# Kernel optimization log

Hardware: AMD Instinct MI355X
Metric: run time of the kernel (lower is better)

## Reference

```python
import jax, jax.numpy as jnp
import numpy as np

N_PF, N_GW, N_SW = 60000, 300000, 60000
D_IN, D, E = 32, 64, 1_000_000


def _mk_edge(key, n_src, n_dst, n_edges):
    k1, k2 = jax.random.split(key)
    return jnp.stack([
        jax.random.randint(k1, (n_edges,), 0, n_src),
        jax.random.randint(k2, (n_edges,), 0, n_dst),
    ]).astype(jnp.int32)


def _self_edge(n):
    r = jnp.arange(n, dtype=jnp.int32)
    return jnp.stack([r, r])


def setup_inputs() -> dict:
    key = jax.random.key(0)
    ks = jax.random.split(key, 20)
    s = 0.05
    return {
        "x_pf": jax.random.normal(ks[0], (N_PF, D_IN), jnp.float32),
        "x_gw": jax.random.normal(ks[1], (N_GW, D_IN), jnp.float32),
        "x_sw": jax.random.normal(ks[2], (N_SW, D_IN), jnp.float32),
        "W1l": jax.random.normal(ks[3], (10, D, D_IN), jnp.float32) * s,
        "b1l": jax.random.normal(ks[4], (10, D), jnp.float32) * s,
        "W1r": jax.random.normal(ks[5], (10, D, D_IN), jnp.float32) * s,
        "W2l": jax.random.normal(ks[6], (10, D, D), jnp.float32) * s,
        "b2l": jax.random.normal(ks[7], (10, D), jnp.float32) * s,
        "W2r": jax.random.normal(ks[8], (10, D, D), jnp.float32) * s,
        "lin_W": jax.random.normal(ks[9], (1, D), jnp.float32) * s,
        "lin_b": jax.random.normal(ks[10], (1,), jnp.float32) * s,
        "prelu_a": jnp.float32(0.25),
        "ei_pf_gw": _mk_edge(ks[11], N_PF, N_GW, E),
        "ei_gw_pf": _mk_edge(ks[12], N_GW, N_PF, E),
        "ei_pf_sw": _mk_edge(ks[13], N_PF, N_SW, E),
        "ei_sw_pf": _mk_edge(ks[14], N_SW, N_PF, E),
        "ei_sw_gw": _mk_edge(ks[15], N_SW, N_GW, E),
        "ei_gw_sw": _mk_edge(ks[16], N_GW, N_SW, E),
        "ei_gw_gw": _mk_edge(ks[17], N_GW, N_GW, E),
        "ei_gw_self": _self_edge(N_GW),
        "ei_sw_self": _self_edge(N_SW),
        "ei_pf_self": _self_edge(N_PF),
    }


def reference(x_pf, x_gw, x_sw, W1l, b1l, W1r, W2l, b2l, W2r, lin_W, lin_b,
              prelu_a, ei_pf_gw, ei_gw_pf, ei_pf_sw, ei_sw_pf, ei_sw_gw,
              ei_gw_sw, ei_gw_gw, ei_gw_self, ei_sw_self, ei_pf_self):
    n_pf, n_gw, n_sw = x_pf.shape[0], x_gw.shape[0], x_sw.shape[0]

    def sage(x_src, x_dst, ei, Wl, bl, Wr, n_dst):
        # PyG SAGEConv: lin_l(mean_j x_j) + lin_r(x_i); lin_r has no bias
        msg = x_src[ei[0]]                                        # [E, Din]
        summed = jax.ops.segment_sum(msg, ei[1], num_segments=n_dst)
        cnt = jax.ops.segment_sum(jnp.ones(ei.shape[1], x_src.dtype), ei[1],
                                  num_segments=n_dst)
        mean = summed / jnp.maximum(cnt, 1.0)[:, None]            # [Ndst, Din]
        return mean @ Wl.T + bl + x_dst @ Wr.T

    def layer(h_pf, h_gw, h_sw, Wl, bl, Wr):
        # HeteroConv with aggr='sum' over edge types per destination node type
        out_gw = (sage(h_pf, h_gw, ei_pf_gw, Wl[0], bl[0], Wr[0], n_gw)
                  + sage(h_sw, h_gw, ei_sw_gw, Wl[4], bl[4], Wr[4], n_gw)
                  + sage(h_gw, h_gw, ei_gw_gw, Wl[6], bl[6], Wr[6], n_gw)
                  + sage(h_gw, h_gw, ei_gw_self, Wl[7], bl[7], Wr[7], n_gw))
        out_pf = (sage(h_gw, h_pf, ei_gw_pf, Wl[1], bl[1], Wr[1], n_pf)
                  + sage(h_sw, h_pf, ei_sw_pf, Wl[3], bl[3], Wr[3], n_pf)
                  + sage(h_pf, h_pf, ei_pf_self, Wl[9], bl[9], Wr[9], n_pf))
        out_sw = (sage(h_pf, h_sw, ei_pf_sw, Wl[2], bl[2], Wr[2], n_sw)
                  + sage(h_gw, h_sw, ei_gw_sw, Wl[5], bl[5], Wr[5], n_sw)
                  + sage(h_sw, h_sw, ei_sw_self, Wl[8], bl[8], Wr[8], n_sw))
        return out_pf, out_gw, out_sw

    h_pf, h_gw, h_sw = layer(x_pf, x_gw, x_sw, W1l, b1l, W1r)
    h_pf, h_gw, h_sw = jax.nn.relu(h_pf), jax.nn.relu(h_gw), jax.nn.relu(h_sw)
    h_pf, h_gw, h_sw = layer(h_pf, h_gw, h_sw, W2l, b2l, W2r)
    h_pf, h_gw, h_sw = jax.nn.relu(h_pf), jax.nn.relu(h_gw), jax.nn.relu(h_sw)

    def prelu(v):
        return jnp.where(v >= 0, v, prelu_a * v)

    out_gw = prelu(h_gw @ lin_W.T + lin_b)   # [N_GW, 1]
    out_sw = prelu(h_sw @ lin_W.T + lin_b)   # [N_SW, 1]
    return out_gw, out_sw, h_pf
```

## Files before the change

### kernel.cpp

```cpp
#include <hip/hip_runtime.h>

typedef __attribute__((ext_vector_type(8))) short short8;
typedef __attribute__((ext_vector_type(4))) float floatx4;

#define N_PF 60000
#define N_GW 300000
#define N_SW 60000
#define EPT 1000000
#define TOTE 7000000
#define L_CNT 1140000
#define SPAN 4096
#define N_B 279
#define CHSZ 4096
#define NCH 1709

__device__ __forceinline__ unsigned short f2bf(float f) {
  unsigned u = __float_as_uint(f);
  u = (u + 0x7FFF + ((u >> 16) & 1)) >> 16;
  return (unsigned short)u;
}
__device__ __forceinline__ float bf2f(unsigned short u) {
  return __uint_as_float((unsigned)u << 16);
}
__device__ __forceinline__ void acc8(float* a, short8 v) {
#pragma unroll
  for (int k = 0; k < 8; ++k) a[k] += bf2f((unsigned short)v[k]);
}

__device__ __forceinline__ int cnt_base(int et) {
  switch (et) {
    case 0: return 0;
    case 1: return 300000;
    case 2: return 360000;
    case 3: return 420000;
    case 4: return 480000;
    case 5: return 780000;
    default: return 840000;
  }
}

__device__ __forceinline__ const int* pick(const int* e0, const int* e1,
                                           const int* e2, const int* e3,
                                           const int* e4, const int* e5,
                                           const int* e6, int et) {
  switch (et) {
    case 0: return e0; case 1: return e1; case 2: return e2; case 3: return e3;
    case 4: return e4; case 5: return e5; default: return e6;
  }
}

__global__ __launch_bounds__(256) void k_cast(const float4* __restrict__ x,
                                              ushort4* __restrict__ xb, int n4) {
  int i = blockIdx.x * 256 + threadIdx.x;
  if (i < n4) {
    float4 v = x[i];
    ushort4 o;
    o.x = f2bf(v.x); o.y = f2bf(v.y); o.z = f2bf(v.z); o.w = f2bf(v.w);
    xb[i] = o;
  }
}


__global__ __launch_bounds__(256) void k_h1(
    const int* e0, const int* e1, const int* e2, const int* e3,
    const int* e4, const int* e5, const int* e6, int* __restrict__ hcnt) {
  __shared__ int hist[N_B];
  int ch = blockIdx.x, t = threadIdx.x;
  for (int i = t; i < N_B; i += 256) hist[i] = 0;
  __syncthreads();
  int base = ch * CHSZ;
  int nn = TOTE - base; if (nn > CHSZ) nn = CHSZ;
#pragma unroll
  for (int u = 0; u < CHSZ / 256; ++u) {
    int o = u * 256 + t;
    if (o < nn) {
      int gid = base + o;
      int et = gid / EPT, i2 = gid - et * EPT;
      const int* ei = pick(e0, e1, e2, e3, e4, e5, e6, et);
      int idx = cnt_base(et) + ei[EPT + i2];
      atomicAdd(&hist[idx >> 12], 1);
    }
  }
  __syncthreads();
  for (int b = t; b < N_B; b += 256) hcnt[(size_t)b * NCH + ch] = hist[b];
}

__global__ __launch_bounds__(256) void k_h2a(const int* __restrict__ hcnt,
                                             int* __restrict__ btot) {
  __shared__ int sh[4];
  int b = blockIdx.x;
  const int* c = hcnt + (size_t)b * NCH;
  int s = 0;
  for (int k = threadIdx.x; k < NCH; k += 256) s += c[k];
  for (int off = 1; off < 64; off <<= 1) s += __shfl_xor(s, off, 64);
  int lane = threadIdx.x & 63, w = threadIdx.x >> 6;
  if (lane == 0) sh[w] = s;
  __syncthreads();
  if (threadIdx.x == 0) btot[b] = sh[0] + sh[1] + sh[2] + sh[3];
}

__global__ __launch_bounds__(64) void k_h2b(const int* __restrict__ btot,
                                            int* __restrict__ bbase,
                                            int* __restrict__ Sarr) {
  int lane = threadIdx.x;
  int v[5]; int s = 0;
#pragma unroll
  for (int k = 0; k < 5; ++k) {
    int i = lane * 5 + k;
    v[k] = (i < N_B) ? btot[i] : 0;
    s += v[k];
  }
  int x = s;
  for (int off = 1; off < 64; off <<= 1) {
    int tv = __shfl_up(x, off, 64);
    if (lane >= off) x += tv;
  }
  int run = x - s;
#pragma unroll
  for (int k = 0; k < 5; ++k) {
    int i = lane * 5 + k;
    if (i < N_B) bbase[i] = run;
    run += v[k];
  }
  if (lane == 63) { bbase[N_B] = x; Sarr[L_CNT] = TOTE; }
}

__global__ __launch_bounds__(256) void k_h2c(int* __restrict__ hcnt,
                                             const int* __restrict__ bbase) {
  __shared__ int sc[256];
  int b = blockIdx.x, t = threadIdx.x;
  int* c = hcnt + (size_t)b * NCH;
  int v[7]; int s = 0;
#pragma unroll
  for (int k = 0; k < 7; ++k) {
    int i = t * 7 + k;
    v[k] = (i < NCH) ? c[i] : 0;
    s += v[k];
  }
  sc[t] = s;
  __syncthreads();
  for (int off = 1; off < 256; off <<= 1) {
    int tv = (t >= off) ? sc[t - off] : 0;
    __syncthreads();
    sc[t] += tv;
    __syncthreads();
  }
  int run = bbase[b] + sc[t] - s;
#pragma unroll
  for (int k = 0; k < 7; ++k) {
    int i = t * 7 + k;
    if (i < NCH) { int vv = v[k]; c[i] = run; run += vv; }
  }
}

__global__ __launch_bounds__(256) void k_bfill(
    const int* e0, const int* e1, const int* e2, const int* e3,
    const int* e4, const int* e5, const int* e6,
    const int* __restrict__ hcnt, unsigned* __restrict__ part) {
  __shared__ int hist[N_B];
  __shared__ int segs[N_B];
  __shared__ int curb[N_B];
  __shared__ int gbase[N_B];
  __shared__ int sc[256];
  __shared__ unsigned long long stg[CHSZ];
  int ch = blockIdx.x, t = threadIdx.x;
  for (int i = t; i < N_B; i += 256) hist[i] = 0;
  __syncthreads();
  int base = ch * CHSZ;
  int nn = TOTE - base; if (nn > CHSZ) nn = CHSZ;
#pragma unroll
  for (int u = 0; u < CHSZ / 256; ++u) {
    int o = u * 256 + t;
    if (o < nn) {
      int gid = base + o;
      int et = gid / EPT, i2 = gid - et * EPT;
      const int* ei = pick(e0, e1, e2, e3, e4, e5, e6, et);
      int idx = cnt_base(et) + ei[EPT + i2];
      atomicAdd(&hist[idx >> 12], 1);
    }
  }
  __syncthreads();
  int v0 = (2 * t < N_B) ? hist[2 * t] : 0;
  int v1 = (2 * t + 1 < N_B) ? hist[2 * t + 1] : 0;
  int s = v0 + v1;
  sc[t] = s;
  __syncthreads();
  for (int off = 1; off < 256; off <<= 1) {
    int tv = (t >= off) ? sc[t - off] : 0;
    __syncthreads();
    sc[t] += tv;
    __syncthreads();
  }
  int excl = sc[t] - s;
  if (2 * t < N_B) { segs[2 * t] = excl; curb[2 * t] = excl; }
  if (2 * t + 1 < N_B) { segs[2 * t + 1] = excl + v0; curb[2 * t + 1] = excl + v0; }
  for (int b = t; b < N_B; b += 256) gbase[b] = hcnt[(size_t)b * NCH + ch];
  __syncthreads();
#pragma unroll
  for (int u = 0; u < CHSZ / 256; ++u) {
    int o = u * 256 + t;
    if (o < nn) {
      int gid = base + o;
      int et = gid / EPT, i2 = gid - et * EPT;
      const int* ei = pick(e0, e1, e2, e3, e4, e5, e6, et);
      int dst = ei[EPT + i2];
      int src = ei[i2];
      int idx = cnt_base(et) + dst;
      unsigned long long p = ((unsigned long long)idx << 32) | (unsigned)src;
      int r = atomicAdd(&curb[idx >> 12], 1);
      stg[r] = p;
    }
  }
  __syncthreads();
  for (int sdx = t; sdx < nn; sdx += 256) {
    unsigned long long p = stg[sdx];
    int idx = (int)(p >> 32);
    int b = idx >> 12;
    unsigned ent = ((unsigned)(idx & 4095) << 19) | (unsigned)(p & 0x7FFFF);
    part[(size_t)gbase[b] + (sdx - segs[b])] = ent;
  }
}

__global__ __launch_bounds__(1024) void k_cfill(
    const unsigned* __restrict__ part, const int* __restrict__ bbase,
    int* __restrict__ Sarr, int* __restrict__ col) {
  __shared__ int hist[SPAN];
  __shared__ int wt[16];
  int t = threadIdx.x;
  int lane = t & 63, wv = t >> 6;
  int b = blockIdx.x;
  int lo = b * SPAN;
  int span_n = L_CNT - lo; if (span_n > SPAN) span_n = SPAN;
  int s0 = bbase[b], s1 = bbase[b + 1];
  ((int4*)hist)[t] = (int4){0, 0, 0, 0};
  __syncthreads();
  for (int j = s0 + t; j < s1; j += 1024) {
    int local = (int)(part[j] >> 19);
    atomicAdd(&hist[local], 1);
  }
  __syncthreads();
  int4 v = ((int4*)hist)[t];
  int s = v.x + v.y + v.z + v.w;
  int x = s;
#pragma unroll
  for (int off = 1; off < 64; off <<= 1) {
    int tv = __shfl_up(x, off, 64);
    if (lane >= off) x += tv;
  }
  if (lane == 63) wt[wv] = x;
  __syncthreads();
  int woff = 0;
#pragma unroll
  for (int k = 0; k < 16; ++k) woff += (k < wv) ? wt[k] : 0;
  int run = woff + x - s;
  int4 cur4, sa4;
  cur4.x = run; sa4.x = s0 + run; run += v.x;
  cur4.y = run; sa4.y = s0 + run; run += v.y;
  cur4.z = run; sa4.z = s0 + run; run += v.z;
  cur4.w = run; sa4.w = s0 + run; run += v.w;
  __syncthreads();
  ((int4*)hist)[t] = cur4;
  if (t * 4 + 3 < span_n) {
    *(int4*)(&Sarr[lo + t * 4]) = sa4;
  } else {
    if (t * 4 + 0 < span_n) Sarr[lo + t * 4 + 0] = sa4.x;
    if (t * 4 + 1 < span_n) Sarr[lo + t * 4 + 1] = sa4.y;
    if (t * 4 + 2 < span_n) Sarr[lo + t * 4 + 2] = sa4.z;
  }
  __syncthreads();
  for (int j = s0 + t; j < s1; j += 1024) {
    unsigned p = part[j];
    int local = (int)(p >> 19);
    int r = atomicAdd(&hist[local], 1);
    col[s0 + r] = (int)(p & 0x7FFFF);
  }
}

template <int KIN, int NE>
__global__ __launch_bounds__(256) void k_prep(
    const float* __restrict__ Wl, const float* __restrict__ Wr,
    const float* __restrict__ bl, int e0, int e1, int e2, int es,
    unsigned short* __restrict__ wsw, float* __restrict__ bias) {
  constexpr int KCAT = (NE + 1) * KIN;
  int idx = blockIdx.x * 256 + threadIdx.x;
  if (idx < KCAT * 64) {
    int j = idx & 7, lane = (idx >> 3) & 63, t = idx >> 9;
    int ct = t & 3, kc = t >> 2;
    int k = kc * 32 + ((lane >> 4) << 3) + j;
    int c = ct * 16 + (lane & 15);
    int seg = k / KIN, kk = k - seg * KIN;
    float v;
    if (seg < NE) {
      int e = (seg == 0) ? e0 : (seg == 1) ? e1 : e2;
      v = Wl[((size_t)e * 64 + c) * KIN + kk];
    } else {
      v = Wl[((size_t)es * 64 + c) * KIN + kk] +
          Wr[((size_t)es * 64 + c) * KIN + kk] +
          Wr[((size_t)e0 * 64 + c) * KIN + kk] +
          Wr[((size_t)e1 * 64 + c) * KIN + kk];
      if (NE == 3) v += Wr[((size_t)e2 * 64 + c) * KIN + kk];
    }
    wsw[idx] = f2bf(v);
  } else if (idx < KCAT * 64 + 64) {
    int c = idx - KCAT * 64;
    float v = bl[e0 * 64 + c] + bl[e1 * 64 + c] + bl[es * 64 + c];
    if (NE == 3) v += bl[e2 * 64 + c];
    bias[c] = v;
  }
}

struct LType {
  const unsigned short* s0;
  const unsigned short* s1;
  const unsigned short* s2;
  int b0, b1, b2, ne;
  const unsigned short* xD;
  const unsigned short* wsw;
  const float* bias;
  void* hOut;
  int omode;
  int ntile;
};

template <int KIN, int MINW>
__global__ __launch_bounds__(256, MINW) void k_layerF(
    const int* __restrict__ Sarr, const int* __restrict__ col, LType t0,
    LType t1, LType t2, const float* __restrict__ linW,
    const float* __restrict__ linb, const float* __restrict__ pa) {
  constexpr int ZSTR = 3 * KIN + 8;
  constexpr int LPR = KIN / 8;
  constexpr int G = 64 / LPR;
  constexpr int KD = KIN / 32;
  __shared__ unsigned short z[4 * 16 * ZSTR];
  const int lane = threadIdx.x & 63;
  unsigned short* zw = &z[(threadIdx.x >> 6) * 16 * ZSTR];
  const int wid = (blockIdx.x * 256 + threadIdx.x) >> 6;
  const int nw = (gridDim.x * 256) >> 6;
  const int cl = lane & 15, quad = lane >> 4;
  const int g = lane / LPR;
  const int c = lane % LPR;
  const int TT = t0.ntile + t1.ntile + t2.ntile;

  for (int tile = wid; tile < TT; tile += nw) {
    LType tp;
    int lt = tile;
    if (lt < t0.ntile) tp = t0;
    else if ((lt -= t0.ntile) < t1.ntile) tp = t1;
    else { lt -= t1.ntile; tp = t2; }
    const int nb = lt * 16;
    const int ne = tp.ne;
    const int klds = ne * KD;

    short8 adst[KD];
#pragma unroll
    for (int kd = 0; kd < KD; ++kd)
      adst[kd] = *(const short8*)(tp.xD + (size_t)(nb + cl) * KIN +
                                  kd * 32 + quad * 8);

#pragma unroll
    for (int i0 = 0; i0 < 16; i0 += G) {
      int n = nb + i0 + g;
      unsigned short* zr = &zw[(i0 + g) * ZSTR];
      int s0v = Sarr[tp.b0 + n], t0v = Sarr[tp.b0 + n + 1];
      int s1v = Sarr[tp.b1 + n], t1v = Sarr[tp.b1 + n + 1];
      int s2v = 0, t2v = 0;
      if (ne == 3) { s2v = Sarr[tp.b2 + n]; t2v = Sarr[tp.b2 + n + 1]; }
#pragma unroll
      for (int E = 0; E < 3; ++E) {
        if (E < ne) {
          const unsigned short* se =
              (E == 0) ? tp.s0 : (E == 1) ? tp.s1 : tp.s2;
          int s = (E == 0) ? s0v : (E == 1) ? s1v : s2v;
          int t = (E == 0) ? t0v : (E == 1) ? t1v : t2v;
          float a0[8] = {0, 0, 0, 0, 0, 0, 0, 0};
          float a1[8] = {0, 0, 0, 0, 0, 0, 0, 0};
          int j = s;
          for (; j + 1 < t; j += 2) {
            int r0 = col[j], r1 = col[j + 1];
            short8 v0 = *(const short8*)(se + (size_t)r0 * KIN + c * 8);
            short8 v1 = *(const short8*)(se + (size_t)r1 * KIN + c * 8);
            acc8(a0, v0);
            acc8(a1, v1);
          }
          if (j < t) {
            int r0 = col[j];
            short8 v0 = *(const short8*)(se + (size_t)r0 * KIN + c * 8);
            acc8(a0, v0);
          }
          int cv = t - s;
          if (cv < 1) cv = 1;
          float inv = 1.0f / (float)cv;
          short8 o;
#pragma unroll
          for (int k = 0; k < 8; ++k)
            o[k] = (short)f2bf((a0[k] + a1[k]) * inv);
          *(short8*)(&zr[E * KIN + c * 8]) = o;
        }
      }
    }
    floatx4 acc[4];
#pragma unroll
    for (int ct = 0; ct < 4; ++ct) {
      float bv = tp.bias[ct * 16 + cl];
      acc[ct] = (floatx4){bv, bv, bv, bv};
    }
    for (int kc = 0; kc < klds; ++kc) {
      short8 a = *(const short8*)(&zw[cl * ZSTR + kc * 32 + quad * 8]);
#pragma unroll
      for (int ct = 0; ct < 4; ++ct) {
        short8 b =
            *(const short8*)(tp.wsw + ((size_t)(kc * 4 + ct) * 64 + lane) * 8);
        acc[ct] = __builtin_amdgcn_mfma_f32_16x16x32_bf16(a, b, acc[ct], 0, 0, 0);
      }
    }
#pragma unroll
    for (int kd = 0; kd < KD; ++kd) {
      short8 a = adst[kd];
      int kc = klds + kd;
#pragma unroll
      for (int ct = 0; ct < 4; ++ct) {
        short8 b =
            *(const short8*)(tp.wsw + ((size_t)(kc * 4 + ct) * 64 + lane) * 8);
        acc[ct] = __builtin_amdgcn_mfma_f32_16x16x32_bf16(a, b, acc[ct], 0, 0, 0);
      }
    }
    if (tp.omode == 2) {
      float p[4] = {0.f, 0.f, 0.f, 0.f};
#pragma unroll
      for (int ct = 0; ct < 4; ++ct) {
        float w = linW[ct * 16 + cl];
#pragma unroll
        for (int r = 0; r < 4; ++r) {
          float v = acc[ct][r];
          v = v > 0.f ? v : 0.f;
          p[r] += v * w;
        }
      }
#pragma unroll
      for (int off = 1; off < 16; off <<= 1) {
#pragma unroll
        for (int r = 0; r < 4; ++r) p[r] += __shfl_xor(p[r], off, 64);
      }
      if (cl == 0) {
        float lb = linb[0], al = pa[0];
        float* o = (float*)tp.hOut;
#pragma unroll
        for (int r = 0; r < 4; ++r) {
          int n = nb + quad * 4 + r;
          float v = p[r] + lb;
          o[n] = v >= 0.f ? v : al * v;
        }
      }
    } else if (tp.omode == 1) {
#pragma unroll
      for (int ct = 0; ct < 4; ++ct)
#pragma unroll
        for (int r = 0; r < 4; ++r) {
          int n = nb + quad * 4 + r;
          float v = acc[ct][r];
          ((float*)tp.hOut)[(size_t)n * 64 + ct * 16 + cl] = v > 0.f ? v : 0.f;
        }
    } else {
#pragma unroll
      for (int ct = 0; ct < 4; ++ct)
#pragma unroll
        for (int r = 0; r < 4; ++r) {
          int n = nb + quad * 4 + r;
          float v = acc[ct][r];
          ((unsigned short*)tp.hOut)[(size_t)n * 64 + ct * 16 + cl] =
              f2bf(v > 0.f ? v : 0.f);
        }
    }
  }
}

extern "C" void kernel_launch(void* const* d_in, const int* in_sizes, int n_in,
                              void* d_out, int out_size, void* d_ws,
                              size_t ws_size, hipStream_t stream) {
  const float* x_pf = (const float*)d_in[0];
  const float* x_gw = (const float*)d_in[1];
  const float* x_sw = (const float*)d_in[2];
  const float* W1l = (const float*)d_in[3];
  const float* b1l = (const float*)d_in[4];
  const float* W1r = (const float*)d_in[5];
  const float* W2l = (const float*)d_in[6];
  const float* b2l = (const float*)d_in[7];
  const float* W2r = (const float*)d_in[8];
  const float* linW = (const float*)d_in[9];
  const float* linb = (const float*)d_in[10];
  const float* pa = (const float*)d_in[11];
  const int* e0 = (const int*)d_in[12];
  const int* e1 = (const int*)d_in[13];
  const int* e2 = (const int*)d_in[14];
  const int* e3 = (const int*)d_in[15];
  const int* e4 = (const int*)d_in[16];
  const int* e5 = (const int*)d_in[17];
  const int* e6 = (const int*)d_in[18];
  float* out = (float*)d_out;

  char* w = (char*)d_ws;
  size_t off = 0;
  auto alloc = [&](size_t bytes) -> void* {
    void* p = w + off;
    off += bytes;
    off = (off + 255) & ~(size_t)255;
    return p;
  };
  unsigned* part = (unsigned*)alloc((size_t)TOTE * 4);
  int* col = (int*)alloc((size_t)TOTE * 4);
  int* Sarr = (int*)alloc((size_t)(L_CNT + 1) * 4);
  int* hcnt = (int*)alloc((size_t)N_B * NCH * 4);
  int* btot = (int*)alloc((N_B + 1) * 4);
  int* bbase = (int*)alloc((N_B + 1) * 4);
  unsigned short* xb_pf = (unsigned short*)alloc((size_t)N_PF * 32 * 2);
  unsigned short* xb_gw = (unsigned short*)alloc((size_t)N_GW * 32 * 2);
  unsigned short* xb_sw = (unsigned short*)alloc((size_t)N_SW * 32 * 2);
  unsigned short* h1_pf = (unsigned short*)alloc((size_t)N_PF * 64 * 2);
  unsigned short* h1_gw = (unsigned short*)alloc((size_t)N_GW * 64 * 2);
  unsigned short* h1_sw = (unsigned short*)alloc((size_t)N_SW * 64 * 2);
  unsigned short* w1gw = (unsigned short*)alloc(128 * 64 * 2);
  unsigned short* w1pf = (unsigned short*)alloc(96 * 64 * 2);
  unsigned short* w1sw = (unsigned short*)alloc(96 * 64 * 2);
  unsigned short* w2gw = (unsigned short*)alloc(256 * 64 * 2);
  unsigned short* w2pf = (unsigned short*)alloc(192 * 64 * 2);
  unsigned short* w2sw = (unsigned short*)alloc(192 * 64 * 2);
  float* bs1gw = (float*)alloc(64 * 4);
  float* bs1pf = (float*)alloc(64 * 4);
  float* bs1sw = (float*)alloc(64 * 4);
  float* bs2gw = (float*)alloc(64 * 4);
  float* bs2pf = (float*)alloc(64 * 4);
  float* bs2sw = (float*)alloc(64 * 4);

  k_cast<<<(N_PF * 8 + 255) / 256, 256, 0, stream>>>((const float4*)x_pf,
                                                     (ushort4*)xb_pf, N_PF * 8);
  k_cast<<<(N_GW * 8 + 255) / 256, 256, 0, stream>>>((const float4*)x_gw,
                                                     (ushort4*)xb_gw, N_GW * 8);
  k_cast<<<(N_SW * 8 + 255) / 256, 256, 0, stream>>>((const float4*)x_sw,
                                                     (ushort4*)xb_sw, N_SW * 8);

  k_h1<<<NCH, 256, 0, stream>>>(e0, e1, e2, e3, e4, e5, e6, hcnt);
  k_h2a<<<N_B, 256, 0, stream>>>(hcnt, btot);
  k_h2b<<<1, 64, 0, stream>>>(btot, bbase, Sarr);
  k_h2c<<<N_B, 256, 0, stream>>>(hcnt, bbase);
  k_bfill<<<NCH, 256, 0, stream>>>(e0, e1, e2, e3, e4, e5, e6, hcnt, part);
  k_cfill<<<N_B, 1024, 0, stream>>>(part, bbase, Sarr, col);

  k_prep<32, 3><<<(128 * 64 + 64 + 255) / 256, 256, 0, stream>>>(
      W1l, W1r, b1l, 0, 4, 6, 7, w1gw, bs1gw);
  k_prep<32, 2><<<(96 * 64 + 64 + 255) / 256, 256, 0, stream>>>(
      W1l, W1r, b1l, 1, 3, 0, 9, w1pf, bs1pf);
  k_prep<32, 2><<<(96 * 64 + 64 + 255) / 256, 256, 0, stream>>>(
      W1l, W1r, b1l, 2, 5, 0, 8, w1sw, bs1sw);
  k_prep<64, 3><<<(256 * 64 + 64 + 255) / 256, 256, 0, stream>>>(
      W2l, W2r, b2l, 0, 4, 6, 7, w2gw, bs2gw);
  k_prep<64, 2><<<(192 * 64 + 64 + 255) / 256, 256, 0, stream>>>(
      W2l, W2r, b2l, 1, 3, 0, 9, w2pf, bs2pf);
  k_prep<64, 2><<<(192 * 64 + 64 + 255) / 256, 256, 0, stream>>>(
      W2l, W2r, b2l, 2, 5, 0, 8, w2sw, bs2sw);

  LType a0{xb_pf, xb_sw, xb_gw, 0, 480000, 840000, 3,
           xb_gw, w1gw, bs1gw, h1_gw, 0, N_GW / 16};
  LType a1{xb_gw, xb_sw, nullptr, 300000, 420000, 0, 2,
           xb_pf, w1pf, bs1pf, h1_pf, 0, N_PF / 16};
  LType a2{xb_pf, xb_gw, nullptr, 360000, 780000, 0, 2,
           xb_sw, w1sw, bs1sw, h1_sw, 0, N_SW / 16};
  k_layerF<32, 8><<<2048, 256, 0, stream>>>(Sarr, col, a0, a1, a2, linW, linb,
                                            pa);

  LType c0{h1_pf, h1_sw, h1_gw, 0, 480000, 840000, 3,
           h1_gw, w2gw, bs2gw, out, 2, N_GW / 16};
  LType c1{h1_gw, h1_sw, nullptr, 300000, 420000, 0, 2,
           h1_pf, w2pf, bs2pf, out + 360000, 1, N_PF / 16};
  LType c2{h1_pf, h1_gw, nullptr, 360000, 780000, 0, 2,
           h1_sw, w2sw, bs2sw, out + N_GW, 2, N_SW / 16};
  k_layerF<64, 6><<<1536, 256, 0, stream>>>(Sarr, col, c0, c1, c2, linW, linb,
                                            pa);
}
```

Before: 677.3 us.

## Aggregate and MFMA per edge type to shrink LDS tile and raise occupancy

The fused layer kernel now processes one incoming edge type at a time: it mean-aggregates into a single-type LDS tile, then immediately runs the MFMAs for that type's weight slice. Previously all three aggregates were staged together before one GEMM. The destination-feature MFMA with bias init is also moved ahead of the aggregation. This cuts the per-wave LDS staging buffer to about a third, and the layer-2 launch is raised to 8 waves per SIMD with a larger grid. The cost is less overlap of gather loads across edge types and more interleaving of gather and MFMA phases.

```diff
diff --git a/kernel.cpp b/kernel.cpp
--- a/kernel.cpp
+++ b/kernel.cpp
@@ -327,7 +327,7 @@
     const int* __restrict__ Sarr, const int* __restrict__ col, LType t0,
     LType t1, LType t2, const float* __restrict__ linW,
     const float* __restrict__ linb, const float* __restrict__ pa) {
-  constexpr int ZSTR = 3 * KIN + 8;
+  constexpr int ZSTR = KIN + 8;
   constexpr int LPR = KIN / 8;
   constexpr int G = 64 / LPR;
   constexpr int KD = KIN / 32;
@@ -351,27 +351,36 @@
     const int ne = tp.ne;
     const int klds = ne * KD;
 
-    short8 adst[KD];
-#pragma unroll
-    for (int kd = 0; kd < KD; ++kd)
-      adst[kd] = *(const short8*)(tp.xD + (size_t)(nb + cl) * KIN +
+    floatx4 acc[4];
+#pragma unroll
+    for (int ct = 0; ct < 4; ++ct) {
+      float bv = tp.bias[ct * 16 + cl];
+      acc[ct] = (floatx4){bv, bv, bv, bv};
+    }
+#pragma unroll
+    for (int kd = 0; kd < KD; ++kd) {
+      short8 a = *(const short8*)(tp.xD + (size_t)(nb + cl) * KIN +
                                   kd * 32 + quad * 8);
-
-#pragma unroll
-    for (int i0 = 0; i0 < 16; i0 += G) {
-      int n = nb + i0 + g;
-      unsigned short* zr = &zw[(i0 + g) * ZSTR];
-      int s0v = Sarr[tp.b0 + n], t0v = Sarr[tp.b0 + n + 1];
-      int s1v = Sarr[tp.b1 + n], t1v = Sarr[tp.b1 + n + 1];
-      int s2v = 0, t2v = 0;
-      if (ne == 3) { s2v = Sarr[tp.b2 + n]; t2v = Sarr[tp.b2 + n + 1]; }
-#pragma unroll
-      for (int E = 0; E < 3; ++E) {
-        if (E < ne) {
-          const unsigned short* se =
-              (E == 0) ? tp.s0 : (E == 1) ? tp.s1 : tp.s2;
-          int s = (E == 0) ? s0v : (E == 1) ? s1v : s2v;
-          int t = (E == 0) ? t0v : (E == 1) ? t1v : t2v;
+      int kc = klds + kd;
+#pragma unroll
+      for (int ct = 0; ct < 4; ++ct) {
+        short8 b =
+            *(const short8*)(tp.wsw + ((size_t)(kc * 4 + ct) * 64 + lane) * 8);
+        acc[ct] = __builtin_amdgcn_mfma_f32_16x16x32_bf16(a, b, acc[ct], 0, 0, 0);
+      }
+    }
+
+#pragma unroll
+    for (int E = 0; E < 3; ++E) {
+      if (E < ne) {
+        const unsigned short* se = (E == 0) ? tp.s0 : (E == 1) ? tp.s1 : tp.s2;
+        int be = (E == 0) ? tp.b0 : (E == 1) ? tp.b1 : tp.b2;
+#pragma unroll
+        for (int i0 = 0; i0 < 16; i0 += G) {
+          int n = nb + i0 + g;
+          unsigned short* zr = &zw[(i0 + g) * ZSTR];
+          int s = Sarr[be + n];
+          int t = Sarr[be + n + 1];
           float a0[8] = {0, 0, 0, 0, 0, 0, 0, 0};
           float a1[8] = {0, 0, 0, 0, 0, 0, 0, 0};
           int j = s;
@@ -394,34 +403,20 @@
 #pragma unroll
           for (int k = 0; k < 8; ++k)
             o[k] = (short)f2bf((a0[k] + a1[k]) * inv);
-          *(short8*)(&zr[E * KIN + c * 8]) = o;
+          *(short8*)(&zr[c * 8]) = o;
         }
-      }
-    }
-    floatx4 acc[4];
-#pragma unroll
-    for (int ct = 0; ct < 4; ++ct) {
-      float bv = tp.bias[ct * 16 + cl];
-      acc[ct] = (floatx4){bv, bv, bv, bv};
-    }
-    for (int kc = 0; kc < klds; ++kc) {
-      short8 a = *(const short8*)(&zw[cl * ZSTR + kc * 32 + quad * 8]);
-#pragma unroll
-      for (int ct = 0; ct < 4; ++ct) {
-        short8 b =
-            *(const short8*)(tp.wsw + ((size_t)(kc * 4 + ct) * 64 + lane) * 8);
-        acc[ct] = __builtin_amdgcn_mfma_f32_16x16x32_bf16(a, b, acc[ct], 0, 0, 0);
-      }
-    }
-#pragma unroll
-    for (int kd = 0; kd < KD; ++kd) {
-      short8 a = adst[kd];
-      int kc = klds + kd;
-#pragma unroll
-      for (int ct = 0; ct < 4; ++ct) {
-        short8 b =
-            *(const short8*)(tp.wsw + ((size_t)(kc * 4 + ct) * 64 + lane) * 8);
-        acc[ct] = __builtin_amdgcn_mfma_f32_16x16x32_bf16(a, b, acc[ct], 0, 0, 0);
+#pragma unroll
+        for (int kc2 = 0; kc2 < KD; ++kc2) {
+          short8 a = *(const short8*)(&zw[cl * ZSTR + kc2 * 32 + quad * 8]);
+          int kc = E * KD + kc2;
+#pragma unroll
+          for (int ct = 0; ct < 4; ++ct) {
+            short8 b = *(const short8*)(tp.wsw +
+                                        ((size_t)(kc * 4 + ct) * 64 + lane) * 8);
+            acc[ct] =
+                __builtin_amdgcn_mfma_f32_16x16x32_bf16(a, b, acc[ct], 0, 0, 0);
+          }
+        }
       }
     }
     if (tp.omode == 2) {
@@ -573,6 +568,6 @@
            h1_pf, w2pf, bs2pf, out + 360000, 1, N_PF / 16};
   LType c2{h1_pf, h1_gw, nullptr, 360000, 780000, 0, 2,
            h1_sw, w2sw, bs2sw, out + N_GW, 2, N_SW / 16};
-  k_layerF<64, 6><<<1536, 256, 0, stream>>>(Sarr, col, c0, c1, c2, linW, linb,
+  k_layerF<64, 8><<<2048, 256, 0, stream>>>(Sarr, col, c0, c1, c2, linW, linb,
                                             pa);
 }
```

Result: slower. 721.8 us (+6.6%).

## Aggregate third edge type in registers in MFMA layout for layer 2

Applied to the files above, without the earlier changes.

For the 64-wide second layer, the third edge segment (gw-gw edges for gateway nodes) is now gathered straight into registers in the MFMA A-fragment layout instead of being staged through shared memory. This shrinks the per-wave LDS tile from three segments to two, which allows raising the minimum waves per EU from 6 to 8 and the grid from 1536 to 2048 blocks. The catch is that the register gather has each lane walk a whole node's edge list serially, so the gather is less parallel per row and may add register pressure at the tighter launch bound.

```diff
diff --git a/kernel.cpp b/kernel.cpp
--- a/kernel.cpp
+++ b/kernel.cpp
@@ -322,12 +322,13 @@
   int ntile;
 };
 
-template <int KIN, int MINW>
+template <int KIN, int MINW, bool REG3>
 __global__ __launch_bounds__(256, MINW) void k_layerF(
     const int* __restrict__ Sarr, const int* __restrict__ col, LType t0,
     LType t1, LType t2, const float* __restrict__ linW,
     const float* __restrict__ linb, const float* __restrict__ pa) {
-  constexpr int ZSTR = 3 * KIN + 8;
+  constexpr int NSEG = REG3 ? 2 : 3;
+  constexpr int ZSTR = NSEG * KIN + 8;
   constexpr int LPR = KIN / 8;
   constexpr int G = 64 / LPR;
   constexpr int KD = KIN / 32;
@@ -350,12 +351,44 @@
     const int nb = lt * 16;
     const int ne = tp.ne;
     const int klds = ne * KD;
+    const int nrow = nb + cl;
 
     short8 adst[KD];
 #pragma unroll
     for (int kd = 0; kd < KD; ++kd)
-      adst[kd] = *(const short8*)(tp.xD + (size_t)(nb + cl) * KIN +
+      adst[kd] = *(const short8*)(tp.xD + (size_t)nrow * KIN +
                                   kd * 32 + quad * 8);
+
+    short8 fr2[KD];
+    if constexpr (REG3) {
+      if (ne == 3) {
+        const unsigned short* se = tp.s2;
+        int s = Sarr[tp.b2 + nrow];
+        int t = Sarr[tp.b2 + nrow + 1];
+        float aa[KD][8];
+#pragma unroll
+        for (int kd = 0; kd < KD; ++kd)
+#pragma unroll
+          for (int k = 0; k < 8; ++k) aa[kd][k] = 0.f;
+        for (int j = s; j < t; ++j) {
+          int r = col[j];
+          const unsigned short* p = se + (size_t)r * KIN + quad * 8;
+#pragma unroll
+          for (int kd = 0; kd < KD; ++kd)
+            acc8(aa[kd], *(const short8*)(p + kd * 32));
+        }
+        int cv = t - s;
+        if (cv < 1) cv = 1;
+        float inv = 1.0f / (float)cv;
+#pragma unroll
+        for (int kd = 0; kd < KD; ++kd) {
+          short8 o;
+#pragma unroll
+          for (int k = 0; k < 8; ++k) o[k] = (short)f2bf(aa[kd][k] * inv);
+          fr2[kd] = o;
+        }
+      }
+    }
 
 #pragma unroll
     for (int i0 = 0; i0 < 16; i0 += G) {
@@ -364,9 +397,11 @@
       int s0v = Sarr[tp.b0 + n], t0v = Sarr[tp.b0 + n + 1];
       int s1v = Sarr[tp.b1 + n], t1v = Sarr[tp.b1 + n + 1];
       int s2v = 0, t2v = 0;
-      if (ne == 3) { s2v = Sarr[tp.b2 + n]; t2v = Sarr[tp.b2 + n + 1]; }
-#pragma unroll
-      for (int E = 0; E < 3; ++E) {
+      if (!REG3 && ne == 3) {
+        s2v = Sarr[tp.b2 + n]; t2v = Sarr[tp.b2 + n + 1];
+      }
+#pragma unroll
+      for (int E = 0; E < NSEG; ++E) {
         if (E < ne) {
           const unsigned short* se =
               (E == 0) ? tp.s0 : (E == 1) ? tp.s1 : tp.s2;
@@ -404,13 +439,38 @@
       float bv = tp.bias[ct * 16 + cl];
       acc[ct] = (floatx4){bv, bv, bv, bv};
     }
-    for (int kc = 0; kc < klds; ++kc) {
-      short8 a = *(const short8*)(&zw[cl * ZSTR + kc * 32 + quad * 8]);
-#pragma unroll
-      for (int ct = 0; ct < 4; ++ct) {
-        short8 b =
-            *(const short8*)(tp.wsw + ((size_t)(kc * 4 + ct) * 64 + lane) * 8);
-        acc[ct] = __builtin_amdgcn_mfma_f32_16x16x32_bf16(a, b, acc[ct], 0, 0, 0);
+#pragma unroll
+    for (int E = 0; E < NSEG; ++E) {
+      if (E < ne) {
+#pragma unroll
+        for (int kd = 0; kd < KD; ++kd) {
+          short8 a = *(const short8*)(&zw[cl * ZSTR + (E * KD + kd) * 32 +
+                                          quad * 8]);
+          int kc = E * KD + kd;
+#pragma unroll
+          for (int ct = 0; ct < 4; ++ct) {
+            short8 b = *(const short8*)(tp.wsw +
+                                        ((size_t)(kc * 4 + ct) * 64 + lane) * 8);
+            acc[ct] =
+                __builtin_amdgcn_mfma_f32_16x16x32_bf16(a, b, acc[ct], 0, 0, 0);
+          }
+        }
+      }
+    }
+    if constexpr (REG3) {
+      if (ne == 3) {
+#pragma unroll
+        for (int kd = 0; kd < KD; ++kd) {
+          short8 a = fr2[kd];
+          int kc = 2 * KD + kd;
+#pragma unroll
+          for (int ct = 0; ct < 4; ++ct) {
+            short8 b = *(const short8*)(tp.wsw +
+                                        ((size_t)(kc * 4 + ct) * 64 + lane) * 8);
+            acc[ct] =
+                __builtin_amdgcn_mfma_f32_16x16x32_bf16(a, b, acc[ct], 0, 0, 0);
+          }
+        }
       }
     }
 #pragma unroll
@@ -564,8 +624,8 @@
            xb_pf, w1pf, bs1pf, h1_pf, 0, N_PF / 16};
   LType a2{xb_pf, xb_gw, nullptr, 360000, 780000, 0, 2,
            xb_sw, w1sw, bs1sw, h1_sw, 0, N_SW / 16};
-  k_layerF<32, 8><<<2048, 256, 0, stream>>>(Sarr, col, a0, a1, a2, linW, linb,
-                                            pa);
+  k_layerF<32, 8, false><<<2048, 256, 0, stream>>>(Sarr, col, a0, a1, a2, linW,
+                                                   linb, pa);
 
   LType c0{h1_pf, h1_sw, h1_gw, 0, 480000, 840000, 3,
            h1_gw, w2gw, bs2gw, out, 2, N_GW / 16};
@@ -573,6 +633,6 @@
            h1_pf, w2pf, bs2pf, out + 360000, 1, N_PF / 16};
   LType c2{h1_pf, h1_gw, nullptr, 360000, 780000, 0, 2,
            h1_sw, w2sw, bs2sw, out + N_GW, 2, N_SW / 16};
-  k_layerF<64, 6><<<1536, 256, 0, stream>>>(Sarr, col, c0, c1, c2, linW, linb,
-                                            pa);
-}
+  k_layerF<64, 8, true><<<2048, 256, 0, stream>>>(Sarr, col, c0, c1, c2, linW,
+                                                  linb, pa);
+}
```

Measured after the change: 712.6 us. 1.05x slower.
